# Kernel tuning notes

Hardware: AMD Instinct MI355X
Metric: run time of the kernel (lower is better)

Reference implementation:

```python
import jax, jax.numpy as jnp
import numpy as np

COUPLING = 0.12
EPS = 1e-08
EMBED_DIM = 16
H = 4
REL_MAX_DIST = 64
PAST_LEN = 524288


def setup_inputs() -> dict:
    key = jax.random.key(0)
    ks = jax.random.split(key, 7)
    return {
        "candidate": jax.random.normal(ks[0], (EMBED_DIM, 2), dtype=jnp.float32),
        "z_past": jax.random.normal(ks[1], (PAST_LEN, EMBED_DIM, 2), dtype=jnp.float32),
        "heads_w": jax.random.normal(ks[2], (H, 2 * EMBED_DIM, 4 * EMBED_DIM), dtype=jnp.float32) * 0.05,
        "heads_b": jax.random.normal(ks[3], (H, 2 * EMBED_DIM), dtype=jnp.float32) * 0.05,
        "out_w": jax.random.normal(ks[4], (2 * EMBED_DIM, H * 2 * EMBED_DIM), dtype=jnp.float32) * 0.05,
        "out_b": jax.random.normal(ks[5], (2 * EMBED_DIM,), dtype=jnp.float32) * 0.05,
        "rel_bias": jax.random.normal(ks[6], (2 * REL_MAX_DIST + 1, 2), dtype=jnp.float32) * 0.02,
        "norm_scale": jnp.ones((1,), dtype=jnp.float32),
        "pos": PAST_LEN,
    }


def reference(candidate, z_past, heads_w, heads_b, out_w, out_b, rel_bias, norm_scale, pos):
    # candidate: [D,2] (real/imag), z_past: [P,D,2]
    P, D = z_past.shape[0], z_past.shape[1]
    # features_c = cat([z_curr_rep, z_past], -1); view_as_real + flatten -> [P, 4D]
    feats = jnp.concatenate(
        [jnp.broadcast_to(candidate[None], (P, D, 2)), z_past], axis=1
    ).reshape(P, 4 * D)
    # 4 small MLP heads, tanh, concat: [P, H, 2D] -> mean over past -> [H*2D]
    h = jnp.tanh(jnp.einsum("pd,hod->pho", feats, heads_w) + heads_b[None])
    combined_mean = h.reshape(P, -1).mean(axis=0)
    out = out_w @ combined_mean + out_b          # [2D]
    mod = out.reshape(D, 2)                      # complex mod as real/imag pair
    # relative positional bias: mean over gathered (clipped) indices
    rel = jnp.arange(pos - P, pos)
    idx = jnp.clip(rel + REL_MAX_DIST, 0, 2 * REL_MAX_DIST)
    bias_mean = rel_bias[idx].mean(axis=0)       # [2]
    # z_new = candidate + COUPLING * (mod + bias_mean)
    z = candidate + COUPLING * (mod + bias_mean[None, :])
    # tanh applied independently to real and imag parts
    z = jnp.tanh(z)
    max_int = jnp.max(jnp.sum(z * z, axis=-1))   # max |z|^2
    scale = norm_scale[0] / jnp.sqrt(max_int + EPS)
    return jnp.where(max_int > 0, z * scale, z)  # [D,2]
```

## Files before the change

kernel.cpp:

```cpp
#include <hip/hip_runtime.h>
#include <hip/hip_bf16.h>
#include <math.h>

#define COUPLING 0.12f
#define EPSV 1e-8f
#define SCALE2L2E 2.8853900817779268f

typedef __attribute__((ext_vector_type(8))) short bf16x8;
typedef __attribute__((ext_vector_type(4))) float f32x4;

__device__ __forceinline__ float tanh_from_e2(float y) {
    float e = __builtin_amdgcn_exp2f(y);
    float r = __builtin_amdgcn_rcpf(1.0f + e);
    return fmaf(-2.0f, r, 1.0f);
}
__device__ __forceinline__ float tanh_fast(float x) {
    return tanh_from_e2(SCALE2L2E * x);
}
__device__ __forceinline__ float sig_e2(float y) {
    float e = __builtin_amdgcn_exp2f(y);
    return __builtin_amdgcn_rcpf(1.0f + e);
}

__device__ __forceinline__ short f2bf(float f) {
    __hip_bfloat16 h = __float2bfloat16(f);
    return __builtin_bit_cast(short, h);
}

__global__ __launch_bounds__(128) void phot_prep(
    const float* __restrict__ heads_w, const float* __restrict__ heads_b,
    const float* __restrict__ cand, float* __restrict__ cpre,
    short* __restrict__ wbf)
{
    const int oh = threadIdx.x;
    const float* wr = heads_w + (size_t)oh * 64;
    float s0 = heads_b[oh], s1 = 0.f, s2 = 0.f, s3 = 0.f;
    #pragma unroll
    for (int k = 0; k < 32; k += 4) {
        s0 = fmaf(wr[k+0], cand[k+0], s0);
        s1 = fmaf(wr[k+1], cand[k+1], s1);
        s2 = fmaf(wr[k+2], cand[k+2], s2);
        s3 = fmaf(wr[k+3], cand[k+3], s3);
    }
    cpre[oh] = SCALE2L2E * ((s0 + s1) + (s2 + s3));
    short* wo = wbf + (size_t)oh * 32;
    #pragma unroll
    for (int k = 0; k < 32; ++k) wo[k] = f2bf(SCALE2L2E * wr[32 + k]);
}

__global__ __launch_bounds__(256, 8) void phot_main(
    const float* __restrict__ z_past,
    const short* __restrict__ wbf,
    const float* __restrict__ cpre_g,
    float* __restrict__ partials,
    int P, int NB)
{
    __shared__ float wacc[128];
    __shared__ __align__(16) unsigned short zb[3][4][512];

    const int tid  = threadIdx.x;
    const int lane = tid & 63;
    const int wv   = tid >> 6;
    const int col  = lane & 15;
    const int kg   = lane >> 4;

    const int g0 = wv * 2, g1 = g0 + 1;
    const bf16x8 bfA = *(const bf16x8*)(wbf + (size_t)(g0 * 16 + col) * 32 + kg * 8);
    const bf16x8 bfB = *(const bf16x8*)(wbf + (size_t)(g1 * 16 + col) * 32 + kg * 8);
    const float  cpA = cpre_g[g0 * 16 + col];
    const float  cpB = cpre_g[g1 * 16 + col];

    f32x4 accA = {0,0,0,0}, accB = {0,0,0,0};

    const int T  = (P + 15) >> 4;
    const int Tf = P >> 4;
    const int b  = blockIdx.x;
    const int K  = (b < T) ? ((T - 1 - b) / NB + 1) : 0;
    const int PH = (K + 3) >> 2;

    const int sr = lane >> 2;
    const int sc = lane & 3;
    const int woff = sr * 32 + ((sc ^ (sr & 3)) << 3);

    const int roff = col * 32 + ((kg ^ (col & 3)) << 3);

    f32x4 preA, preB;

    #define SLOADP(ph) { \
        const int j_ = 4 * (ph) + wv; \
        if (j_ < K) { \
            const int tt_ = b + j_ * NB; \
            int grow = tt_ * 16 + sr; if (grow > P - 1) grow = P - 1; \
            const float* g_ = z_past + (size_t)grow * 32 + sc * 8; \
            preA = *(const f32x4*)g_; \
            preB = *(const f32x4*)(g_ + 4); \
        } }
    #define SWRITEP(ph) { \
        const int j_ = 4 * (ph) + wv; \
        if (j_ < K) { \
            bf16x8 w_; \
            w_[0]=f2bf(preA[0]); w_[1]=f2bf(preA[1]); w_[2]=f2bf(preA[2]); w_[3]=f2bf(preA[3]); \
            w_[4]=f2bf(preB[0]); w_[5]=f2bf(preB[1]); w_[6]=f2bf(preB[2]); w_[7]=f2bf(preB[3]); \
            *(bf16x8*)(&zb[(ph) % 3][wv][woff]) = w_; \
        } }
    #define CTILE(p, j) { \
        const int jj_ = 4 * (p) + (j); \
        if (jj_ < K) { \
            const int tt_ = b + jj_ * NB; \
            const bf16x8 a_ = *(const bf16x8*)(&zb[(p) % 3][j][roff]); \
            const int base_ = tt_ * 16; \
            if (base_ + 16 <= P) { \
                f32x4 c_ = {cpA, cpA, cpA, cpA}; \
                f32x4 d_ = __builtin_amdgcn_mfma_f32_16x16x32_bf16(a_, bfA, c_, 0, 0, 0); \
                accA[0] += sig_e2(d_[0]); accA[1] += sig_e2(d_[1]); \
                accA[2] += sig_e2(d_[2]); accA[3] += sig_e2(d_[3]); \
                c_ = {cpB, cpB, cpB, cpB}; \
                d_ = __builtin_amdgcn_mfma_f32_16x16x32_bf16(a_, bfB, c_, 0, 0, 0); \
                accB[0] += sig_e2(d_[0]); accB[1] += sig_e2(d_[1]); \
                accB[2] += sig_e2(d_[2]); accB[3] += sig_e2(d_[3]); \
            } else { \
                const int r0_ = base_ + kg * 4; \
                f32x4 c_ = {cpA, cpA, cpA, cpA}; \
                f32x4 d_ = __builtin_amdgcn_mfma_f32_16x16x32_bf16(a_, bfA, c_, 0, 0, 0); \
                if (r0_ + 0 < P) accA[0] += sig_e2(d_[0]); \
                if (r0_ + 1 < P) accA[1] += sig_e2(d_[1]); \
                if (r0_ + 2 < P) accA[2] += sig_e2(d_[2]); \
                if (r0_ + 3 < P) accA[3] += sig_e2(d_[3]); \
                c_ = {cpB, cpB, cpB, cpB}; \
                d_ = __builtin_amdgcn_mfma_f32_16x16x32_bf16(a_, bfB, c_, 0, 0, 0); \
                if (r0_ + 0 < P) accB[0] += sig_e2(d_[0]); \
                if (r0_ + 1 < P) accB[1] += sig_e2(d_[1]); \
                if (r0_ + 2 < P) accB[2] += sig_e2(d_[2]); \
                if (r0_ + 3 < P) accB[3] += sig_e2(d_[3]); \
            } \
        } }

    if (K > 0) {
        SLOADP(0);
        SWRITEP(0);
        SLOADP(1);
        asm volatile("s_waitcnt lgkmcnt(0)" ::: "memory");
        __builtin_amdgcn_s_barrier();

        for (int p = 0; p < PH; ++p) {
            if (p + 1 < PH) SWRITEP(p + 1);
            if (p + 2 < PH) SLOADP(p + 2);
            CTILE(p, 0); CTILE(p, 1); CTILE(p, 2); CTILE(p, 3);
            asm volatile("s_waitcnt lgkmcnt(0)" ::: "memory");
            __builtin_amdgcn_s_barrier();
        }
    }
    #undef SLOADP
    #undef SWRITEP
    #undef CTILE

    float nsum = 0.0f;
    if (K > 0) {
        int nfull = (b < Tf) ? ((Tf - 1 - b) / NB + 1) : 0;
        nsum = 4.0f * (float)nfull;
        if (Tf < T && b <= Tf && ((Tf - b) % NB) == 0) {
            int prem = P - Tf * 16;
            int nv = prem - kg * 4; if (nv < 0) nv = 0; if (nv > 4) nv = 4;
            nsum += (float)nv;
        }
    }

    float sA = nsum - 2.0f * ((accA[0] + accA[1]) + (accA[2] + accA[3]));
    sA += __shfl_xor(sA, 16, 64);
    sA += __shfl_xor(sA, 32, 64);
    float sB = nsum - 2.0f * ((accB[0] + accB[1]) + (accB[2] + accB[3]));
    sB += __shfl_xor(sB, 16, 64);
    sB += __shfl_xor(sB, 32, 64);
    if (lane < 16) {
        wacc[g0 * 16 + lane] = sA;
        wacc[g1 * 16 + lane] = sB;
    }
    __syncthreads();
    if (tid < 128) {
        partials[(size_t)b * 128 + tid] = wacc[tid];
    }
}

__global__ __launch_bounds__(128) void phot_mid(
    const float* __restrict__ partials, float* __restrict__ mid, int nblk)
{
    const int g = blockIdx.x, t = threadIdx.x;
    const int seg = nblk >> 7, rem = nblk & 127;
    const int b0  = g * seg + (g < rem ? g : rem);
    const int cnt = seg + (g < rem ? 1 : 0);
    const float* p0 = partials + (size_t)b0 * 128 + t;
    float s = 0.f;
    for (int i = 0; i < cnt; ++i) s += p0[(size_t)i * 128];
    mid[(size_t)g * 128 + t] = s;
}

__global__ __launch_bounds__(1024) void phot_finalize(
    const float* __restrict__ partials, int nblk, int P,
    const float* __restrict__ out_w,
    const float* __restrict__ out_b,
    const float* __restrict__ rel_bias,
    const float* __restrict__ cand,
    const float* __restrict__ norm_scale,
    const int* __restrict__ posp,
    float* __restrict__ out)
{
    __shared__ float  sh[1024];
    __shared__ float  cm[128];
    __shared__ float  outv[32];
    __shared__ double db[512];
    __shared__ float  bm[2];

    const int t  = threadIdx.x;
    const int oh = t & 127;
    const int sl = t >> 7;

    const int seg = nblk >> 3;
    const int b0  = sl * seg;
    float a0=0.f,a1=0.f,a2=0.f,a3=0.f,a4=0.f,a5=0.f,a6=0.f,a7=0.f;
    int i = 0;
    for (; i + 8 <= seg; i += 8) {
        const float* pp = partials + (size_t)(b0 + i) * 128 + oh;
        a0 += pp[0*128]; a1 += pp[1*128]; a2 += pp[2*128]; a3 += pp[3*128];
        a4 += pp[4*128]; a5 += pp[5*128]; a6 += pp[6*128]; a7 += pp[7*128];
    }
    for (; i < seg; ++i) a0 += partials[(size_t)(b0 + i) * 128 + oh];
    sh[t] = ((a0+a1)+(a2+a3)) + ((a4+a5)+(a6+a7));
    __syncthreads();

    if (t < 128) {
        float s = 0.0f;
        #pragma unroll
        for (int s2 = 0; s2 < 8; ++s2) s += sh[t + 128*s2];
        cm[t] = s / (float)P;
    }

    if (t < 512) {
        const int c = t >> 8, j = t & 255;
        double v = 0.0;
        if (j <= 128) {
            const long long pos = (long long)(*posp);
            const long long a = pos - (long long)P + 64;
            double cnt;
            if (j == 0) {
                long long hi = -a; if (hi > (long long)P - 1) hi = (long long)P - 1;
                cnt = (hi >= 0) ? (double)(hi + 1) : 0.0;
            } else if (j == 128) {
                long long lo = 128 - a; if (lo < 0) lo = 0;
                cnt = (lo <= (long long)P - 1) ? (double)((long long)P - lo) : 0.0;
            } else {
                long long p = (long long)j - a;
                cnt = (p >= 0 && p < (long long)P) ? 1.0 : 0.0;
            }
            v = cnt * (double)rel_bias[2*j + c];
        }
        db[t] = v;
    }
    __syncthreads();
    #pragma unroll
    for (int s = 128; s >= 1; s >>= 1) {
        if (t < 512 && (t & 255) < s) db[t] += db[t + s];
        __syncthreads();
    }
    if (t < 2) bm[t] = (float)(db[t << 8] / (double)P);
    __syncthreads();

    if (t < 32) {
        const float* wr = out_w + t * 128;
        float o0 = out_b[t], o1 = 0.f, o2 = 0.f, o3 = 0.f;
        #pragma unroll
        for (int j = 0; j < 128; j += 4) {
            o0 = fmaf(wr[j+0], cm[j+0], o0);
            o1 = fmaf(wr[j+1], cm[j+1], o1);
            o2 = fmaf(wr[j+2], cm[j+2], o2);
            o3 = fmaf(wr[j+3], cm[j+3], o3);
        }
        outv[t] = (o0+o1) + (o2+o3);
    }
    __syncthreads();

    if (t < 32) {
        float zt = tanh_fast(cand[t] + COUPLING * (outv[t] + bm[t & 1]));
        float other = __shfl_xor(zt, 1, 64);
        float m = fmaf(zt, zt, other * other);
        #pragma unroll
        for (int off = 2; off < 32; off <<= 1) m = fmaxf(m, __shfl_xor(m, off, 64));
        float scale = norm_scale[0] / sqrtf(m + EPSV);
        out[t] = (m > 0.0f) ? zt * scale : zt;
    }
}

extern "C" void kernel_launch(void* const* d_in, const int* in_sizes, int n_in,
                              void* d_out, int out_size, void* d_ws, size_t ws_size,
                              hipStream_t stream)
{
    const float* cand       = (const float*)d_in[0];
    const float* z_past     = (const float*)d_in[1];
    const float* heads_w    = (const float*)d_in[2];
    const float* heads_b    = (const float*)d_in[3];
    const float* out_w      = (const float*)d_in[4];
    const float* out_b      = (const float*)d_in[5];
    const float* rel_bias   = (const float*)d_in[6];
    const float* norm_scale = (const float*)d_in[7];
    const int*   posp       = (const int*)d_in[8];

    const int P = in_sizes[1] / 32;

    int nblk = 2048;
    size_t need = ((size_t)nblk * 128 + 128 * 128 + 128) * sizeof(float)
                + 128 * 32 * sizeof(short);
    if (need > ws_size) {
        nblk = (int)((ws_size - (128 * 128 + 128) * sizeof(float)
                      - 128 * 32 * sizeof(short)) / (128 * sizeof(float)));
        nblk &= ~7;
        if (nblk < 8) nblk = 8;
    }
    float* partials = (float*)d_ws;
    float* mid      = partials + (size_t)nblk * 128;
    float* cpre     = mid + 128 * 128;
    short* wbf      = (short*)(cpre + 128);

    phot_prep<<<1, 128, 0, stream>>>(heads_w, heads_b, cand, cpre, wbf);
    phot_main<<<nblk, 256, 0, stream>>>(z_past, wbf, cpre, partials, P, nblk);
    phot_mid<<<128, 128, 0, stream>>>(partials, mid, nblk);
    phot_finalize<<<1, 1024, 0, stream>>>(mid, 128, P, out_w, out_b,
                                          rel_bias, cand, norm_scale, posp,
                                          (float*)d_out);
}
```

Before: 39.00 us.

## Deepen global-load prefetch to three register stages with four LDS buffers

The main kernel now keeps three sets of prefetch registers so global loads of z_past are issued three phases ahead instead of two, with a fourth LDS staging buffer and a loop manually unrolled by three. Occupancy hint drops from 8 to 4 waves per SIMD and grid size is halved to 1024 blocks, so each block processes more tiles. The aim is to hide HBM latency better through more loads in flight per wave. The cost is more registers, more shared memory, and lower occupancy. The SWRITEP calls inside the unrolled loop are not bounds-guarded by PH, but they are guarded by j_<K, so they stay safe.

```diff
diff --git a/kernel.cpp b/kernel.cpp
--- a/kernel.cpp
+++ b/kernel.cpp
@@ -48,7 +48,7 @@
     for (int k = 0; k < 32; ++k) wo[k] = f2bf(SCALE2L2E * wr[32 + k]);
 }
 
-__global__ __launch_bounds__(256, 8) void phot_main(
+__global__ __launch_bounds__(256, 4) void phot_main(
     const float* __restrict__ z_past,
     const short* __restrict__ wbf,
     const float* __restrict__ cpre_g,
@@ -56,7 +56,7 @@
     int P, int NB)
 {
     __shared__ float wacc[128];
-    __shared__ __align__(16) unsigned short zb[3][4][512];
+    __shared__ __align__(16) unsigned short zb[4][4][512];
 
     const int tid  = threadIdx.x;
     const int lane = tid & 63;
@@ -84,30 +84,34 @@
 
     const int roff = col * 32 + ((kg ^ (col & 3)) << 3);
 
-    f32x4 preA, preB;
-
-    #define SLOADP(ph) { \
+    f32x4 preA0 = {0,0,0,0}, preB0 = {0,0,0,0};
+    f32x4 preA1 = {0,0,0,0}, preB1 = {0,0,0,0};
+    f32x4 preA2 = {0,0,0,0}, preB2 = {0,0,0,0};
+
+    #define SLOADP(ph, S) { \
         const int j_ = 4 * (ph) + wv; \
         if (j_ < K) { \
             const int tt_ = b + j_ * NB; \
             int grow = tt_ * 16 + sr; if (grow > P - 1) grow = P - 1; \
             const float* g_ = z_past + (size_t)grow * 32 + sc * 8; \
-            preA = *(const f32x4*)g_; \
-            preB = *(const f32x4*)(g_ + 4); \
+            preA##S = *(const f32x4*)g_; \
+            preB##S = *(const f32x4*)(g_ + 4); \
         } }
-    #define SWRITEP(ph) { \
+    #define SWRITEP(ph, S) { \
         const int j_ = 4 * (ph) + wv; \
         if (j_ < K) { \
             bf16x8 w_; \
-            w_[0]=f2bf(preA[0]); w_[1]=f2bf(preA[1]); w_[2]=f2bf(preA[2]); w_[3]=f2bf(preA[3]); \
-            w_[4]=f2bf(preB[0]); w_[5]=f2bf(preB[1]); w_[6]=f2bf(preB[2]); w_[7]=f2bf(preB[3]); \
-            *(bf16x8*)(&zb[(ph) % 3][wv][woff]) = w_; \
+            w_[0]=f2bf(preA##S[0]); w_[1]=f2bf(preA##S[1]); \
+            w_[2]=f2bf(preA##S[2]); w_[3]=f2bf(preA##S[3]); \
+            w_[4]=f2bf(preB##S[0]); w_[5]=f2bf(preB##S[1]); \
+            w_[6]=f2bf(preB##S[2]); w_[7]=f2bf(preB##S[3]); \
+            *(bf16x8*)(&zb[(ph) & 3][wv][woff]) = w_; \
         } }
     #define CTILE(p, j) { \
         const int jj_ = 4 * (p) + (j); \
         if (jj_ < K) { \
             const int tt_ = b + jj_ * NB; \
-            const bf16x8 a_ = *(const bf16x8*)(&zb[(p) % 3][j][roff]); \
+            const bf16x8 a_ = *(const bf16x8*)(&zb[(p) & 3][j][roff]); \
             const int base_ = tt_ * 16; \
             if (base_ + 16 <= P) { \
                 f32x4 c_ = {cpA, cpA, cpA, cpA}; \
@@ -135,24 +139,36 @@
             } \
         } }
 
+    #define SYNC { asm volatile("s_waitcnt lgkmcnt(0)" ::: "memory"); \
+                   __builtin_amdgcn_s_barrier(); }
+
     if (K > 0) {
-        SLOADP(0);
-        SWRITEP(0);
-        SLOADP(1);
-        asm volatile("s_waitcnt lgkmcnt(0)" ::: "memory");
-        __builtin_amdgcn_s_barrier();
-
-        for (int p = 0; p < PH; ++p) {
-            if (p + 1 < PH) SWRITEP(p + 1);
-            if (p + 2 < PH) SLOADP(p + 2);
-            CTILE(p, 0); CTILE(p, 1); CTILE(p, 2); CTILE(p, 3);
-            asm volatile("s_waitcnt lgkmcnt(0)" ::: "memory");
-            __builtin_amdgcn_s_barrier();
+        SLOADP(0, 0) SLOADP(1, 1) SLOADP(2, 2)
+        SWRITEP(0, 0)
+        SYNC
+
+        for (int p = 0; p < PH; p += 3) {
+            {
+                SLOADP(p + 3, 0) SWRITEP(p + 1, 1)
+                CTILE(p, 0) CTILE(p, 1) CTILE(p, 2) CTILE(p, 3)
+                SYNC
+            }
+            if (p + 1 < PH) {
+                SLOADP(p + 4, 1) SWRITEP(p + 2, 2)
+                CTILE(p + 1, 0) CTILE(p + 1, 1) CTILE(p + 1, 2) CTILE(p + 1, 3)
+                SYNC
+            }
+            if (p + 2 < PH) {
+                SLOADP(p + 5, 2) SWRITEP(p + 3, 0)
+                CTILE(p + 2, 0) CTILE(p + 2, 1) CTILE(p + 2, 2) CTILE(p + 2, 3)
+                SYNC
+            }
         }
     }
     #undef SLOADP
     #undef SWRITEP
     #undef CTILE
+    #undef SYNC
 
     float nsum = 0.0f;
     if (K > 0) {
@@ -305,7 +321,7 @@
 
     const int P = in_sizes[1] / 32;
 
-    int nblk = 2048;
+    int nblk = 1024;
     size_t need = ((size_t)nblk * 128 + 128 * 128 + 128) * sizeof(float)
                 + 128 * 32 * sizeof(short);
     if (need > ws_size) {
```

Result: slower. 40.79 us (+4.6%).

## Fold prep into main kernel, drop mid reduction, halve block count

Applied to the files above, without the earlier changes.

Each main-kernel block now computes the candidate pre-activation and bf16 head weights into LDS itself, removing the separate single-block prep launch. The intermediate mid-reduction kernel is removed, and finalize reduces all partials directly with vectorized float4 loads across 32 slices. The grid drops from 2048 to 1024 blocks and the occupancy hint from 8 to 4. This trades two launches and their serialization for redundant per-block prep work and a heavier single-block final reduction.

```diff
diff --git a/kernel.cpp b/kernel.cpp
--- a/kernel.cpp
+++ b/kernel.cpp
@@ -27,35 +27,17 @@
     return __builtin_bit_cast(short, h);
 }
 
-__global__ __launch_bounds__(128) void phot_prep(
-    const float* __restrict__ heads_w, const float* __restrict__ heads_b,
-    const float* __restrict__ cand, float* __restrict__ cpre,
-    short* __restrict__ wbf)
-{
-    const int oh = threadIdx.x;
-    const float* wr = heads_w + (size_t)oh * 64;
-    float s0 = heads_b[oh], s1 = 0.f, s2 = 0.f, s3 = 0.f;
-    #pragma unroll
-    for (int k = 0; k < 32; k += 4) {
-        s0 = fmaf(wr[k+0], cand[k+0], s0);
-        s1 = fmaf(wr[k+1], cand[k+1], s1);
-        s2 = fmaf(wr[k+2], cand[k+2], s2);
-        s3 = fmaf(wr[k+3], cand[k+3], s3);
-    }
-    cpre[oh] = SCALE2L2E * ((s0 + s1) + (s2 + s3));
-    short* wo = wbf + (size_t)oh * 32;
-    #pragma unroll
-    for (int k = 0; k < 32; ++k) wo[k] = f2bf(SCALE2L2E * wr[32 + k]);
-}
-
-__global__ __launch_bounds__(256, 8) void phot_main(
+__global__ __launch_bounds__(256, 4) void phot_main(
     const float* __restrict__ z_past,
-    const short* __restrict__ wbf,
-    const float* __restrict__ cpre_g,
+    const float* __restrict__ heads_w,
+    const float* __restrict__ heads_b,
+    const float* __restrict__ cand,
     float* __restrict__ partials,
     int P, int NB)
 {
     __shared__ float wacc[128];
+    __shared__ float cpre_l[128];
+    __shared__ __align__(16) unsigned short wbf_l[128][32];
     __shared__ __align__(16) unsigned short zb[3][4][512];
 
     const int tid  = threadIdx.x;
@@ -64,11 +46,28 @@
     const int col  = lane & 15;
     const int kg   = lane >> 4;
 
+    if (tid < 128) {
+        const float* wr = heads_w + (size_t)tid * 64;
+        float s0 = heads_b[tid], s1 = 0.f, s2 = 0.f, s3 = 0.f;
+        #pragma unroll
+        for (int k = 0; k < 32; k += 4) {
+            s0 = fmaf(wr[k+0], cand[k+0], s0);
+            s1 = fmaf(wr[k+1], cand[k+1], s1);
+            s2 = fmaf(wr[k+2], cand[k+2], s2);
+            s3 = fmaf(wr[k+3], cand[k+3], s3);
+        }
+        cpre_l[tid] = SCALE2L2E * ((s0 + s1) + (s2 + s3));
+        #pragma unroll
+        for (int k = 0; k < 32; ++k)
+            wbf_l[tid][k] = (unsigned short)f2bf(SCALE2L2E * wr[32 + k]);
+    }
+    __syncthreads();
+
     const int g0 = wv * 2, g1 = g0 + 1;
-    const bf16x8 bfA = *(const bf16x8*)(wbf + (size_t)(g0 * 16 + col) * 32 + kg * 8);
-    const bf16x8 bfB = *(const bf16x8*)(wbf + (size_t)(g1 * 16 + col) * 32 + kg * 8);
-    const float  cpA = cpre_g[g0 * 16 + col];
-    const float  cpB = cpre_g[g1 * 16 + col];
+    const bf16x8 bfA = *(const bf16x8*)&wbf_l[g0 * 16 + col][kg * 8];
+    const bf16x8 bfB = *(const bf16x8*)&wbf_l[g1 * 16 + col][kg * 8];
+    const float  cpA = cpre_l[g0 * 16 + col];
+    const float  cpB = cpre_l[g1 * 16 + col];
 
     f32x4 accA = {0,0,0,0}, accB = {0,0,0,0};
 
@@ -135,24 +134,26 @@
             } \
         } }
 
+    #define SYNC { asm volatile("s_waitcnt lgkmcnt(0)" ::: "memory"); \
+                   __builtin_amdgcn_s_barrier(); }
+
     if (K > 0) {
-        SLOADP(0);
-        SWRITEP(0);
-        SLOADP(1);
-        asm volatile("s_waitcnt lgkmcnt(0)" ::: "memory");
-        __builtin_amdgcn_s_barrier();
+        SLOADP(0)
+        SWRITEP(0)
+        SLOADP(1)
+        SYNC
 
         for (int p = 0; p < PH; ++p) {
             if (p + 1 < PH) SWRITEP(p + 1);
             if (p + 2 < PH) SLOADP(p + 2);
-            CTILE(p, 0); CTILE(p, 1); CTILE(p, 2); CTILE(p, 3);
-            asm volatile("s_waitcnt lgkmcnt(0)" ::: "memory");
-            __builtin_amdgcn_s_barrier();
+            CTILE(p, 0) CTILE(p, 1) CTILE(p, 2) CTILE(p, 3)
+            SYNC
         }
     }
     #undef SLOADP
     #undef SWRITEP
     #undef CTILE
+    #undef SYNC
 
     float nsum = 0.0f;
     if (K > 0) {
@@ -179,19 +180,6 @@
     if (tid < 128) {
         partials[(size_t)b * 128 + tid] = wacc[tid];
     }
-}
-
-__global__ __launch_bounds__(128) void phot_mid(
-    const float* __restrict__ partials, float* __restrict__ mid, int nblk)
-{
-    const int g = blockIdx.x, t = threadIdx.x;
-    const int seg = nblk >> 7, rem = nblk & 127;
-    const int b0  = g * seg + (g < rem ? g : rem);
-    const int cnt = seg + (g < rem ? 1 : 0);
-    const float* p0 = partials + (size_t)b0 * 128 + t;
-    float s = 0.f;
-    for (int i = 0; i < cnt; ++i) s += p0[(size_t)i * 128];
-    mid[(size_t)g * 128 + t] = s;
 }
 
 __global__ __launch_bounds__(1024) void phot_finalize(
@@ -204,33 +192,35 @@
     const int* __restrict__ posp,
     float* __restrict__ out)
 {
-    __shared__ float  sh[1024];
+    __shared__ __align__(16) float sh[4096];
     __shared__ float  cm[128];
     __shared__ float  outv[32];
     __shared__ double db[512];
     __shared__ float  bm[2];
 
-    const int t  = threadIdx.x;
-    const int oh = t & 127;
-    const int sl = t >> 7;
-
-    const int seg = nblk >> 3;
-    const int b0  = sl * seg;
-    float a0=0.f,a1=0.f,a2=0.f,a3=0.f,a4=0.f,a5=0.f,a6=0.f,a7=0.f;
+    const int t   = threadIdx.x;
+    const int chg = t & 31;
+    const int sl  = t >> 5;
+
+    const int cnt = nblk >> 5;
+    const float* p0 = partials + (size_t)(sl * cnt) * 128 + chg * 4;
+    f32x4 a0 = {0,0,0,0}, a1 = {0,0,0,0}, a2 = {0,0,0,0}, a3 = {0,0,0,0};
     int i = 0;
-    for (; i + 8 <= seg; i += 8) {
-        const float* pp = partials + (size_t)(b0 + i) * 128 + oh;
-        a0 += pp[0*128]; a1 += pp[1*128]; a2 += pp[2*128]; a3 += pp[3*128];
-        a4 += pp[4*128]; a5 += pp[5*128]; a6 += pp[6*128]; a7 += pp[7*128];
-    }
-    for (; i < seg; ++i) a0 += partials[(size_t)(b0 + i) * 128 + oh];
-    sh[t] = ((a0+a1)+(a2+a3)) + ((a4+a5)+(a6+a7));
+    for (; i + 4 <= cnt; i += 4) {
+        a0 += *(const f32x4*)(p0 + (size_t)(i+0) * 128);
+        a1 += *(const f32x4*)(p0 + (size_t)(i+1) * 128);
+        a2 += *(const f32x4*)(p0 + (size_t)(i+2) * 128);
+        a3 += *(const f32x4*)(p0 + (size_t)(i+3) * 128);
+    }
+    for (; i < cnt; ++i) a0 += *(const f32x4*)(p0 + (size_t)i * 128);
+    f32x4 acc = (a0 + a1) + (a2 + a3);
+    *(f32x4*)&sh[sl * 128 + chg * 4] = acc;
     __syncthreads();
 
     if (t < 128) {
         float s = 0.0f;
         #pragma unroll
-        for (int s2 = 0; s2 < 8; ++s2) s += sh[t + 128*s2];
+        for (int s2 = 0; s2 < 32; ++s2) s += sh[t + 128 * s2];
         cm[t] = s / (float)P;
     }
 
@@ -240,18 +230,18 @@
         if (j <= 128) {
             const long long pos = (long long)(*posp);
             const long long a = pos - (long long)P + 64;
-            double cnt;
+            double cnt2;
             if (j == 0) {
                 long long hi = -a; if (hi > (long long)P - 1) hi = (long long)P - 1;
-                cnt = (hi >= 0) ? (double)(hi + 1) : 0.0;
+                cnt2 = (hi >= 0) ? (double)(hi + 1) : 0.0;
             } else if (j == 128) {
                 long long lo = 128 - a; if (lo < 0) lo = 0;
-                cnt = (lo <= (long long)P - 1) ? (double)((long long)P - lo) : 0.0;
+                cnt2 = (lo <= (long long)P - 1) ? (double)((long long)P - lo) : 0.0;
             } else {
                 long long p = (long long)j - a;
-                cnt = (p >= 0 && p < (long long)P) ? 1.0 : 0.0;
+                cnt2 = (p >= 0 && p < (long long)P) ? 1.0 : 0.0;
             }
-            v = cnt * (double)rel_bias[2*j + c];
+            v = cnt2 * (double)rel_bias[2*j + c];
         }
         db[t] = v;
     }
@@ -305,24 +295,18 @@
 
     const int P = in_sizes[1] / 32;
 
-    int nblk = 2048;
-    size_t need = ((size_t)nblk * 128 + 128 * 128 + 128) * sizeof(float)
-                + 128 * 32 * sizeof(short);
+    int nblk = 1024;
+    size_t need = (size_t)nblk * 128 * sizeof(float);
     if (need > ws_size) {
-        nblk = (int)((ws_size - (128 * 128 + 128) * sizeof(float)
-                      - 128 * 32 * sizeof(short)) / (128 * sizeof(float)));
-        nblk &= ~7;
-        if (nblk < 8) nblk = 8;
+        nblk = (int)(ws_size / (128 * sizeof(float)));
+        nblk &= ~31;
+        if (nblk < 32) nblk = 32;
     }
     float* partials = (float*)d_ws;
-    float* mid      = partials + (size_t)nblk * 128;
-    float* cpre     = mid + 128 * 128;
-    short* wbf      = (short*)(cpre + 128);
-
-    phot_prep<<<1, 128, 0, stream>>>(heads_w, heads_b, cand, cpre, wbf);
-    phot_main<<<nblk, 256, 0, stream>>>(z_past, wbf, cpre, partials, P, nblk);
-    phot_mid<<<128, 128, 0, stream>>>(partials, mid, nblk);
-    phot_finalize<<<1, 1024, 0, stream>>>(mid, 128, P, out_w, out_b,
+
+    phot_main<<<nblk, 256, 0, stream>>>(z_past, heads_w, heads_b, cand,
+                                        partials, P, nblk);
+    phot_finalize<<<1, 1024, 0, stream>>>(partials, nblk, P, out_w, out_b,
                                           rel_bias, cand, norm_scale, posp,
                                           (float*)d_out);
 }
```

Measured after the change: 37.63 us. 3.5% less time.
